# Kernel optimization log

Hardware: AMD Instinct MI355X
Metric: run time of the kernel (lower is better)

## Reference

```python
import jax, jax.numpy as jnp
import numpy as np

B, N, Mc, K = 8, 16384, 2048, 32
EMB = 256


def setup_inputs() -> dict:
    key = jax.random.key(0)
    ks = jax.random.split(key, 9)
    xyz = jax.random.normal(ks[0], (B, N, 3), dtype=jnp.float32)
    centers = jax.random.normal(ks[1], (B, Mc, 3), dtype=jnp.float32)
    idx_knn = jax.random.randint(ks[2], (B, Mc, K), 0, N, dtype=jnp.int32)
    # 1x1 conv weights == pointwise linear layers (out_ch, in_ch) + bias
    def kaiming(k, o, i):
        return jax.random.normal(k, (o, i), dtype=jnp.float32) * np.float32(np.sqrt(2.0 / i))
    W1, b1 = kaiming(ks[3], 64, 3), jnp.zeros((64,), jnp.float32)
    W2, b2 = kaiming(ks[4], 128, 64), jnp.zeros((128,), jnp.float32)
    W3, b3 = kaiming(ks[5], EMB, 128), jnp.zeros((EMB,), jnp.float32)
    return {"xyz": xyz, "centers": centers, "idx_knn": idx_knn,
            "W1": W1, "b1": b1, "W2": W2, "b2": b2, "W3": W3, "b3": b3}


def reference(xyz, centers, idx_knn, W1, b1, W2, b2, W3, b3):
    # gather KNN neighbors: (B, M, K, 3)
    neigh = jnp.take_along_axis(xyz[:, None, :, :], idx_knn[..., None], axis=2)
    local = neigh - centers[:, :, None, :]          # center-subtract
    # 1x1 convs are pointwise linears over the channel dim
    h = jax.nn.relu(jnp.einsum('bmkc,oc->bmko', local, W1) + b1)
    h = jax.nn.relu(jnp.einsum('bmkc,oc->bmko', h, W2) + b2)
    h = jnp.einsum('bmkc,oc->bmko', h, W3) + b3      # (B, M, K, EMB)
    return jnp.max(h, axis=2)                        # max over K -> (B, M, EMB)
```

## Files before the change

### kernel.cpp

```cpp
#include <hip/hip_runtime.h>
#include <hip/hip_bf16.h>


typedef __attribute__((ext_vector_type(8))) short bf16x8;
typedef __attribute__((ext_vector_type(4))) float f32x4v;

constexpr int Bn = 8, Nn = 16384, Mn = 2048, Kn = 32, EMB = 256;
constexpr int G = 2;
constexpr int ROWS = G * Kn;
constexpr int GRID = 1024;
constexpr int ITERS = (Bn * Mn) / G / GRID;

__device__ __forceinline__ unsigned pk2(float a, float b) {
    float2 f; f.x = a; f.y = b;
    __hip_bfloat162 h = __float22bfloat162_rn(f);
    return *(unsigned*)&h;
}

__device__ __forceinline__ bf16x8 pack8(const float* v) {
    unsigned u0 = pk2(v[0], v[1]), u1 = pk2(v[2], v[3]);
    unsigned u2 = pk2(v[4], v[5]), u3 = pk2(v[6], v[7]);
    uint4 u = make_uint4(u0, u1, u2, u3);
    return *(bf16x8*)&u;
}

__global__ __launch_bounds__(256) void pe_pack(
    const float* __restrict__ W2, const float* __restrict__ W3,
    uint4* __restrict__ ws)
{
    int gid = blockIdx.x * 256 + threadIdx.x;
    if (gid < 1024) {
        int e = gid, l = e & 63;
        int kt = (e >> 6) & 1, ct = (e >> 7) & 1, w = e >> 8;
        int q = l >> 4, n = l & 15;
        int ch = w * 32 + ct * 16 + n;
        const float* p = W2 + ch * 64 + kt * 32 + q * 8;
        float t[8];
        *(float4*)&t[0] = *(const float4*)p;
        *(float4*)&t[4] = *(const float4*)(p + 4);
        bf16x8 v = pack8(t);
        ws[e] = *(uint4*)&v;
    } else if (gid < 5120) {
        int e = gid - 1024, l = e & 63;
        int kt = (e >> 6) & 3, ct = (e >> 8) & 3, w = e >> 10;
        int q = l >> 4, n = l & 15;
        int ch = w * 64 + ct * 16 + n;
        const float* p = W3 + ch * 128 + kt * 32 + q * 8;
        float t[8];
        *(float4*)&t[0] = *(const float4*)p;
        *(float4*)&t[4] = *(const float4*)(p + 4);
        bf16x8 v = pack8(t);
        ws[1024 + e] = *(uint4*)&v;
    }
}

__global__ __launch_bounds__(256, 4) void pe_mfma(
    const float* __restrict__ xyz,
    const float* __restrict__ centers,
    const int*   __restrict__ idx,
    const float* __restrict__ W1,
    const float* __restrict__ b1,
    const float* __restrict__ b2,
    const float* __restrict__ b3,
    const uint4* __restrict__ wsf,
    float*       __restrict__ out)
{
    __shared__ uint4 h1v[ROWS * 64 * 2 / 16];
    __shared__ uint4 h2v[ROWS * 128 * 2 / 16];

    const int tid = threadIdx.x;
    const int w   = tid >> 6;
    const int l   = tid & 63;
    const int q   = l >> 4;
    const int n   = l & 15;

    bf16x8 B2f[2][2];
    float4 bb2[2];
    const int ch0 = w * 32 + q * 4;
    #pragma unroll
    for (int ct = 0; ct < 2; ++ct) {
        bb2[ct] = *(const float4*)&b2[ch0 + ct * 16];
        #pragma unroll
        for (int kt = 0; kt < 2; ++kt) {
            uint4 u = wsf[((w * 2 + ct) * 2 + kt) * 64 + l];
            B2f[ct][kt] = *(bf16x8*)&u;
        }
    }
    bf16x8 B3f[4][4];  float b3v[4];
    #pragma unroll
    for (int ct = 0; ct < 4; ++ct) {
        b3v[ct] = b3[w * 64 + ct * 16 + n];
        #pragma unroll
        for (int kt = 0; kt < 4; ++kt) {
            uint4 u = wsf[1024 + ((w * 4 + ct) * 4 + kt) * 64 + l];
            B3f[ct][kt] = *(bf16x8*)&u;
        }
    }
    const int o4b = __builtin_amdgcn_readfirstlane((tid >> 6) * 4);
    float4 W1a[4], W1b[4], W1w[4], b1c[4];
    #pragma unroll
    for (int i = 0; i < 4; ++i) {
        const float4* Wp = (const float4*)(W1 + (o4b + i) * 12);
        W1a[i] = Wp[0]; W1b[i] = Wp[1]; W1w[i] = Wp[2];
        b1c[i] = *(const float4*)(b1 + (o4b + i) * 4);
    }

    const int r64 = tid & 63;
    const int T = r64 >> 4, rr = r64 & 15, j0 = (tid >> 6) * 2;

    #pragma unroll 1
    for (int it = 0; it < ITERS; ++it) {
        const int bm0 = (blockIdx.x + it * GRID) * G;

        int bm = bm0 + (r64 >> 5);
        int bb = bm >> 11;
        int id = idx[(size_t)bm * Kn + (r64 & 31)];
        const float* p = xyz + ((size_t)bb * Nn + id) * 3;
        const float* c = centers + (size_t)bm * 3;
        float lx = p[0] - c[0], ly = p[1] - c[1], lz = p[2] - c[2];

        {
            float h[16];
            #pragma unroll
            for (int i = 0; i < 4; ++i) {
                h[4*i+0] = fmaxf(b1c[i].x + lx*W1a[i].x + ly*W1a[i].y + lz*W1a[i].z, 0.f);
                h[4*i+1] = fmaxf(b1c[i].y + lx*W1a[i].w + ly*W1b[i].x + lz*W1b[i].y, 0.f);
                h[4*i+2] = fmaxf(b1c[i].z + lx*W1b[i].z + ly*W1b[i].w + lz*W1w[i].x, 0.f);
                h[4*i+3] = fmaxf(b1c[i].w + lx*W1w[i].y + ly*W1w[i].z + lz*W1w[i].w, 0.f);
            }
            #pragma unroll
            for (int jj = 0; jj < 2; ++jj) {
                bf16x8 v = pack8(&h[8 * jj]);
                h1v[T * 128 + (j0 + jj) * 16 + rr] = *(uint4*)&v;
            }
        }
        __syncthreads();

        {
            ushort* h2s = (ushort*)h2v;
            #pragma unroll
            for (int rt = 0; rt < G * 2; ++rt) {
                uint4 a0u = h1v[rt * 128 + q * 16 + n];
                uint4 a1u = h1v[rt * 128 + (4 + q) * 16 + n];
                bf16x8 A0 = *(bf16x8*)&a0u, A1 = *(bf16x8*)&a1u;
                #pragma unroll
                for (int ct = 0; ct < 2; ++ct) {
                    int ch = ch0 + ct * 16;
                    f32x4v c0 = {0.f, 0.f, 0.f, 0.f};
                    c0 = __builtin_amdgcn_mfma_f32_16x16x32_bf16(B2f[ct][0], A0, c0, 0, 0, 0);
                    c0 = __builtin_amdgcn_mfma_f32_16x16x32_bf16(B2f[ct][1], A1, c0, 0, 0, 0);
                    unsigned p0 = pk2(fmaxf(c0[0] + bb2[ct].x, 0.f),
                                      fmaxf(c0[1] + bb2[ct].y, 0.f));
                    unsigned p1 = pk2(fmaxf(c0[2] + bb2[ct].z, 0.f),
                                      fmaxf(c0[3] + bb2[ct].w, 0.f));
                    uint2 pk; pk.x = p0; pk.y = p1;
                    *(uint2*)&h2s[rt * 2048 + (ch >> 3) * 128 + n * 8 + (ch & 7)] = pk;
                }
            }
        }
        __syncthreads();

        {
            #pragma unroll
            for (int g = 0; g < G; ++g) {
                bf16x8 Ae[4], Ao[4];
                #pragma unroll
                for (int kt = 0; kt < 4; ++kt) {
                    uint4 ae = h2v[(2*g)   * 256 + (kt * 4 + q) * 16 + n];
                    uint4 ao = h2v[(2*g+1) * 256 + (kt * 4 + q) * 16 + n];
                    Ae[kt] = *(bf16x8*)&ae;
                    Ao[kt] = *(bf16x8*)&ao;
                }
                #pragma unroll
                for (int ct = 0; ct < 4; ++ct) {
                    f32x4v Ce = {0.f, 0.f, 0.f, 0.f};
                    f32x4v Co = {0.f, 0.f, 0.f, 0.f};
                    #pragma unroll
                    for (int kt = 0; kt < 4; ++kt) {
                        Ce = __builtin_amdgcn_mfma_f32_16x16x32_bf16(Ae[kt], B3f[ct][kt], Ce, 0, 0, 0);
                        Co = __builtin_amdgcn_mfma_f32_16x16x32_bf16(Ao[kt], B3f[ct][kt], Co, 0, 0, 0);
                    }
                    float v = fmaxf(fmaxf(fmaxf(Ce[0], Co[0]), fmaxf(Ce[1], Co[1])),
                                    fmaxf(fmaxf(Ce[2], Co[2]), fmaxf(Ce[3], Co[3])));
                    v = fmaxf(v, __shfl_xor(v, 16));
                    v = fmaxf(v, __shfl_xor(v, 32));
                    if (q == 0) {
                        out[(size_t)(bm0 + g) * EMB + w * 64 + ct * 16 + n] = v + b3v[ct];
                    }
                }
            }
        }
    }
}

extern "C" void kernel_launch(void* const* d_in, const int* in_sizes, int n_in,
                              void* d_out, int out_size, void* d_ws, size_t ws_size,
                              hipStream_t stream) {
    const float* xyz     = (const float*)d_in[0];
    const float* centers = (const float*)d_in[1];
    const int*   idx     = (const int*)  d_in[2];
    const float* W1      = (const float*)d_in[3];
    const float* b1      = (const float*)d_in[4];
    const float* W2      = (const float*)d_in[5];
    const float* b2      = (const float*)d_in[6];
    const float* W3      = (const float*)d_in[7];
    const float* b3      = (const float*)d_in[8];
    float*       out     = (float*)d_out;
    uint4*       ws      = (uint4*)d_ws;

    pe_pack<<<20, 256, 0, stream>>>(W2, W3, ws);
    pe_mfma<<<GRID, 256, 0, stream>>>(
        xyz, centers, idx, W1, b1, b2, b3, ws, out);
}
```

Measured before the change: 147.3 us.

## Switch to 32x32x16 MFMA tiles and launch one block per center pair

Replaces the 16x16x32 bf16 MFMA tiling with 32x32x16 MFMAs for both the 64->128 and 128->256 layers. The weight pre-pack layout and the LDS layouts for the intermediate activations are reorganised to match the new fragment shapes. The persistent loop over 1024 blocks is removed, so the kernel now launches 8192 blocks that each handle two centers. The larger tiles cut instruction count and shuffle reductions, but every block now reloads the weight fragments from global memory, adding launch and per-block setup overhead.

```diff
diff --git a/kernel.cpp b/kernel.cpp
--- a/kernel.cpp
+++ b/kernel.cpp
@@ -2,14 +2,12 @@
 #include <hip/hip_bf16.h>
 
 
-typedef __attribute__((ext_vector_type(8))) short bf16x8;
-typedef __attribute__((ext_vector_type(4))) float f32x4v;
+typedef __attribute__((ext_vector_type(8)))  short bf16x8;
+typedef __attribute__((ext_vector_type(16))) float f32x16;
 
 constexpr int Bn = 8, Nn = 16384, Mn = 2048, Kn = 32, EMB = 256;
 constexpr int G = 2;
 constexpr int ROWS = G * Kn;
-constexpr int GRID = 1024;
-constexpr int ITERS = (Bn * Mn) / G / GRID;
 
 __device__ __forceinline__ unsigned pk2(float a, float b) {
     float2 f; f.x = a; f.y = b;
@@ -31,10 +29,8 @@
     int gid = blockIdx.x * 256 + threadIdx.x;
     if (gid < 1024) {
         int e = gid, l = e & 63;
-        int kt = (e >> 6) & 1, ct = (e >> 7) & 1, w = e >> 8;
-        int q = l >> 4, n = l & 15;
-        int ch = w * 32 + ct * 16 + n;
-        const float* p = W2 + ch * 64 + kt * 32 + q * 8;
+        int kt = (e >> 6) & 3, mt = e >> 8;
+        const float* p = W2 + (mt * 32 + (l & 31)) * 64 + kt * 16 + (l >> 5) * 8;
         float t[8];
         *(float4*)&t[0] = *(const float4*)p;
         *(float4*)&t[4] = *(const float4*)(p + 4);
@@ -42,10 +38,8 @@
         ws[e] = *(uint4*)&v;
     } else if (gid < 5120) {
         int e = gid - 1024, l = e & 63;
-        int kt = (e >> 6) & 3, ct = (e >> 8) & 3, w = e >> 10;
-        int q = l >> 4, n = l & 15;
-        int ch = w * 64 + ct * 16 + n;
-        const float* p = W3 + ch * 128 + kt * 32 + q * 8;
+        int kk = (e >> 6) & 7, nt = e >> 9;
+        const float* p = W3 + (nt * 32 + (l & 31)) * 128 + kk * 16 + (l >> 5) * 8;
         float t[8];
         *(float4*)&t[0] = *(const float4*)p;
         *(float4*)&t[4] = *(const float4*)(p + 4);
@@ -65,38 +59,39 @@
     const uint4* __restrict__ wsf,
     float*       __restrict__ out)
 {
-    __shared__ uint4 h1v[ROWS * 64 * 2 / 16];
-    __shared__ uint4 h2v[ROWS * 128 * 2 / 16];
+    __shared__ uint4 h1v[2 * 4 * 64];
+    __shared__ uint4 h2v[2 * 8 * 64];
 
     const int tid = threadIdx.x;
     const int w   = tid >> 6;
     const int l   = tid & 63;
-    const int q   = l >> 4;
-    const int n   = l & 15;
-
-    bf16x8 B2f[2][2];
-    float4 bb2[2];
-    const int ch0 = w * 32 + q * 4;
-    #pragma unroll
-    for (int ct = 0; ct < 2; ++ct) {
-        bb2[ct] = *(const float4*)&b2[ch0 + ct * 16];
-        #pragma unroll
-        for (int kt = 0; kt < 2; ++kt) {
-            uint4 u = wsf[((w * 2 + ct) * 2 + kt) * 64 + l];
-            B2f[ct][kt] = *(bf16x8*)&u;
-        }
-    }
-    bf16x8 B3f[4][4];  float b3v[4];
-    #pragma unroll
-    for (int ct = 0; ct < 4; ++ct) {
-        b3v[ct] = b3[w * 64 + ct * 16 + n];
-        #pragma unroll
-        for (int kt = 0; kt < 4; ++kt) {
-            uint4 u = wsf[1024 + ((w * 4 + ct) * 4 + kt) * 64 + l];
-            B3f[ct][kt] = *(bf16x8*)&u;
-        }
-    }
-    const int o4b = __builtin_amdgcn_readfirstlane((tid >> 6) * 4);
+    const int hl  = l >> 5;
+    const int bm0 = blockIdx.x * G;
+
+    bf16x8 A2[4];
+    #pragma unroll
+    for (int kt = 0; kt < 4; ++kt) {
+        uint4 u = wsf[(w * 4 + kt) * 64 + l];
+        A2[kt] = *(bf16x8*)&u;
+    }
+    bf16x8 B3[2][8];
+    float  b3v[2];
+    #pragma unroll
+    for (int c2 = 0; c2 < 2; ++c2) {
+        int nt = w + 4 * c2;
+        b3v[c2] = b3[nt * 32 + (l & 31)];
+        #pragma unroll
+        for (int kk = 0; kk < 8; ++kk) {
+            uint4 u = wsf[1024 + (nt * 8 + kk) * 64 + l];
+            B3[c2][kk] = *(bf16x8*)&u;
+        }
+    }
+    float4 bb2[4];
+    #pragma unroll
+    for (int t = 0; t < 4; ++t)
+        bb2[t] = *(const float4*)&b2[32 * w + 8 * t + 4 * hl];
+
+    const int o4b = __builtin_amdgcn_readfirstlane(w * 4);
     float4 W1a[4], W1b[4], W1w[4], b1c[4];
     #pragma unroll
     for (int i = 0; i < 4; ++i) {
@@ -105,88 +100,84 @@
         b1c[i] = *(const float4*)(b1 + (o4b + i) * 4);
     }
 
-    const int r64 = tid & 63;
-    const int T = r64 >> 4, rr = r64 & 15, j0 = (tid >> 6) * 2;
-
-    #pragma unroll 1
-    for (int it = 0; it < ITERS; ++it) {
-        const int bm0 = (blockIdx.x + it * GRID) * G;
-
-        int bm = bm0 + (r64 >> 5);
+    const int r = l;
+    {
+        int bm = bm0 + (r >> 5);
         int bb = bm >> 11;
-        int id = idx[(size_t)bm * Kn + (r64 & 31)];
+        int id = idx[(size_t)bm * Kn + (r & 31)];
         const float* p = xyz + ((size_t)bb * Nn + id) * 3;
         const float* c = centers + (size_t)bm * 3;
         float lx = p[0] - c[0], ly = p[1] - c[1], lz = p[2] - c[2];
 
-        {
-            float h[16];
-            #pragma unroll
-            for (int i = 0; i < 4; ++i) {
-                h[4*i+0] = fmaxf(b1c[i].x + lx*W1a[i].x + ly*W1a[i].y + lz*W1a[i].z, 0.f);
-                h[4*i+1] = fmaxf(b1c[i].y + lx*W1a[i].w + ly*W1b[i].x + lz*W1b[i].y, 0.f);
-                h[4*i+2] = fmaxf(b1c[i].z + lx*W1b[i].z + ly*W1b[i].w + lz*W1w[i].x, 0.f);
-                h[4*i+3] = fmaxf(b1c[i].w + lx*W1w[i].y + ly*W1w[i].z + lz*W1w[i].w, 0.f);
-            }
-            #pragma unroll
-            for (int jj = 0; jj < 2; ++jj) {
-                bf16x8 v = pack8(&h[8 * jj]);
-                h1v[T * 128 + (j0 + jj) * 16 + rr] = *(uint4*)&v;
-            }
-        }
-        __syncthreads();
-
-        {
-            ushort* h2s = (ushort*)h2v;
-            #pragma unroll
-            for (int rt = 0; rt < G * 2; ++rt) {
-                uint4 a0u = h1v[rt * 128 + q * 16 + n];
-                uint4 a1u = h1v[rt * 128 + (4 + q) * 16 + n];
-                bf16x8 A0 = *(bf16x8*)&a0u, A1 = *(bf16x8*)&a1u;
+        float h[16];
+        #pragma unroll
+        for (int i = 0; i < 4; ++i) {
+            h[4*i+0] = fmaxf(b1c[i].x + lx*W1a[i].x + ly*W1a[i].y + lz*W1a[i].z, 0.f);
+            h[4*i+1] = fmaxf(b1c[i].y + lx*W1a[i].w + ly*W1b[i].x + lz*W1b[i].y, 0.f);
+            h[4*i+2] = fmaxf(b1c[i].z + lx*W1b[i].z + ly*W1b[i].w + lz*W1w[i].x, 0.f);
+            h[4*i+3] = fmaxf(b1c[i].w + lx*W1w[i].y + ly*W1w[i].z + lz*W1w[i].w, 0.f);
+        }
+        #pragma unroll
+        for (int hh = 0; hh < 2; ++hh) {
+            bf16x8 v = pack8(&h[8 * hh]);
+            h1v[((r >> 5) * 4 + w) * 64 + (r & 31) + 32 * hh] = *(uint4*)&v;
+        }
+    }
+    __syncthreads();
+
+    {
+        #pragma unroll
+        for (int rt2 = 0; rt2 < 2; ++rt2) {
+            f32x16 C;
+            #pragma unroll
+            for (int i = 0; i < 16; ++i) C[i] = 0.f;
+            #pragma unroll
+            for (int kt = 0; kt < 4; ++kt) {
+                uint4 u = h1v[(rt2 * 4 + kt) * 64 + l];
+                C = __builtin_amdgcn_mfma_f32_32x32x16_bf16(A2[kt], *(bf16x8*)&u, C, 0, 0, 0);
+            }
+            #pragma unroll
+            for (int t = 0; t < 4; ++t) {
+                unsigned p0 = pk2(fmaxf(C[4*t+0] + bb2[t].x, 0.f),
+                                  fmaxf(C[4*t+1] + bb2[t].y, 0.f));
+                unsigned p1 = pk2(fmaxf(C[4*t+2] + bb2[t].z, 0.f),
+                                  fmaxf(C[4*t+3] + bb2[t].w, 0.f));
+                uint2 pk; pk.x = p0; pk.y = p1;
+                ushort* dst = (ushort*)h2v
+                    + (((rt2 * 8 + 2 * w + (t >> 1)) * 64 + (l & 31) + 32 * (t & 1)) * 8
+                       + 4 * hl);
+                *(uint2*)dst = pk;
+            }
+        }
+    }
+    __syncthreads();
+
+    {
+        #pragma unroll
+        for (int rt2 = 0; rt2 < 2; ++rt2) {
+            bf16x8 Af[8];
+            #pragma unroll
+            for (int kk = 0; kk < 8; ++kk) {
+                uint4 u = h2v[(rt2 * 8 + kk) * 64 + l];
+                Af[kk] = *(bf16x8*)&u;
+            }
+            #pragma unroll
+            for (int c2 = 0; c2 < 2; ++c2) {
+                f32x16 C;
                 #pragma unroll
-                for (int ct = 0; ct < 2; ++ct) {
-                    int ch = ch0 + ct * 16;
-                    f32x4v c0 = {0.f, 0.f, 0.f, 0.f};
-                    c0 = __builtin_amdgcn_mfma_f32_16x16x32_bf16(B2f[ct][0], A0, c0, 0, 0, 0);
-                    c0 = __builtin_amdgcn_mfma_f32_16x16x32_bf16(B2f[ct][1], A1, c0, 0, 0, 0);
-                    unsigned p0 = pk2(fmaxf(c0[0] + bb2[ct].x, 0.f),
-                                      fmaxf(c0[1] + bb2[ct].y, 0.f));
-                    unsigned p1 = pk2(fmaxf(c0[2] + bb2[ct].z, 0.f),
-                                      fmaxf(c0[3] + bb2[ct].w, 0.f));
-                    uint2 pk; pk.x = p0; pk.y = p1;
-                    *(uint2*)&h2s[rt * 2048 + (ch >> 3) * 128 + n * 8 + (ch & 7)] = pk;
-                }
-            }
-        }
-        __syncthreads();
-
-        {
-            #pragma unroll
-            for (int g = 0; g < G; ++g) {
-                bf16x8 Ae[4], Ao[4];
+                for (int i = 0; i < 16; ++i) C[i] = 0.f;
                 #pragma unroll
-                for (int kt = 0; kt < 4; ++kt) {
-                    uint4 ae = h2v[(2*g)   * 256 + (kt * 4 + q) * 16 + n];
-                    uint4 ao = h2v[(2*g+1) * 256 + (kt * 4 + q) * 16 + n];
-                    Ae[kt] = *(bf16x8*)&ae;
-                    Ao[kt] = *(bf16x8*)&ao;
-                }
-                #pragma unroll
-                for (int ct = 0; ct < 4; ++ct) {
-                    f32x4v Ce = {0.f, 0.f, 0.f, 0.f};
-                    f32x4v Co = {0.f, 0.f, 0.f, 0.f};
-                    #pragma unroll
-                    for (int kt = 0; kt < 4; ++kt) {
-                        Ce = __builtin_amdgcn_mfma_f32_16x16x32_bf16(Ae[kt], B3f[ct][kt], Ce, 0, 0, 0);
-                        Co = __builtin_amdgcn_mfma_f32_16x16x32_bf16(Ao[kt], B3f[ct][kt], Co, 0, 0, 0);
-                    }
-                    float v = fmaxf(fmaxf(fmaxf(Ce[0], Co[0]), fmaxf(Ce[1], Co[1])),
-                                    fmaxf(fmaxf(Ce[2], Co[2]), fmaxf(Ce[3], Co[3])));
-                    v = fmaxf(v, __shfl_xor(v, 16));
-                    v = fmaxf(v, __shfl_xor(v, 32));
-                    if (q == 0) {
-                        out[(size_t)(bm0 + g) * EMB + w * 64 + ct * 16 + n] = v + b3v[ct];
-                    }
+                for (int kk = 0; kk < 8; ++kk)
+                    C = __builtin_amdgcn_mfma_f32_32x32x16_bf16(Af[kk], B3[c2][kk], C, 0, 0, 0);
+                float m0 = fmaxf(fmaxf(C[0],  C[1]),  fmaxf(C[2],  C[3]));
+                float m1 = fmaxf(fmaxf(C[4],  C[5]),  fmaxf(C[6],  C[7]));
+                float m2 = fmaxf(fmaxf(C[8],  C[9]),  fmaxf(C[10], C[11]));
+                float m3 = fmaxf(fmaxf(C[12], C[13]), fmaxf(C[14], C[15]));
+                float v  = fmaxf(fmaxf(m0, m1), fmaxf(m2, m3));
+                v = fmaxf(v, __shfl_xor(v, 32));
+                if (l < 32) {
+                    int nt = w + 4 * c2;
+                    out[(size_t)(bm0 + rt2) * EMB + nt * 32 + l] = v + b3v[c2];
                 }
             }
         }
@@ -209,6 +200,6 @@
     uint4*       ws      = (uint4*)d_ws;
 
     pe_pack<<<20, 256, 0, stream>>>(W2, W3, ws);
-    pe_mfma<<<GRID, 256, 0, stream>>>(
+    pe_mfma<<<(Bn * Mn) / G, 256, 0, stream>>>(
         xyz, centers, idx, W1, b1, b2, b3, ws, out);
 }
```

New measurement: 122.2 us. 1.21x faster.
